# Performance work log

Measured on AMD Instinct MI355X. Metric: run time of the kernel, lower is better.

Reference implementation:

```python
import jax, jax.numpy as jnp
import numpy as np

S, N, E = 2048, 8, 512
C = 1024          # tot_classes
G = 32            # num_groups
CG = C // G       # classes_per_group = 32
INTERP_PROB = 1.0
LN_EPS = 1e-5


def setup_inputs() -> dict:
    key = jax.random.key(0)
    ks = jax.random.split(key, 8)
    return {
        "x": jax.random.normal(ks[0], (S, N, E), jnp.float32),
        "W1": jax.random.normal(ks[1], (C, E), jnp.float32) * 0.02,
        "b1": jnp.zeros((C,), jnp.float32),
        "class_offsets": jnp.zeros((C,), jnp.float32),
        "W2": jax.random.normal(ks[2], (E, C), jnp.float32) * 0.02,
        "b2": jnp.zeros((E,), jnp.float32),
        "ln_gamma": jnp.ones((E,), jnp.float32),
        "ln_beta": jnp.zeros((E,), jnp.float32),
        # Gumbel noise for the two categorical draws per group
        "g1": jax.random.gumbel(ks[3], (S, N, G, CG), jnp.float32),
        "g2": jax.random.gumbel(ks[4], (S, N, G, CG), jnp.float32),
        # interpolation weight and interp-decision uniform
        "w_interp": jax.random.uniform(ks[5], (S, N, G), jnp.float32),
        "u_interp": jax.random.uniform(ks[6], (S, N, G), jnp.float32),
    }


def _layer_norm(h, gamma, beta):
    mu = jnp.mean(h, axis=-1, keepdims=True)
    var = jnp.mean(jnp.square(h - mu), axis=-1, keepdims=True)
    return (h - mu) * jax.lax.rsqrt(var + LN_EPS) * gamma + beta


def reference(x, W1, b1, class_offsets, W2, b2, ln_gamma, ln_beta,
              g1, g2, w_interp, u_interp):
    # linear1, *3 scale, + class_offsets (min_prob_ratio > 0 path)
    logits = (jnp.einsum('sne,ce->snc', x, W1) + b1) * 3.0 + class_offsets
    lg = logits.reshape(S, N, G, CG)                      # grouped logits
    soft = jax.nn.softmax(lg, axis=-1)                    # per-group softmax
    softmax_out = soft.reshape(S, N, C)
    # flow_sample with straight_through_scale == 1.0:
    # categorical sample (Gumbel-argmax) of two classes, interpolate with
    # prob interp_prob, straight-through derivatives from the softmax.
    logp = jax.nn.log_softmax(lg, axis=-1)
    oh_i = jax.nn.one_hot(jnp.argmax(logp + g1, axis=-1), CG, dtype=lg.dtype)
    oh_j = jax.nn.one_hot(jnp.argmax(logp + g2, axis=-1), CG, dtype=lg.dtype)
    w = w_interp[..., None]
    interp = w * oh_i + (1.0 - w) * oh_j                  # E[interp] = softmax
    hard = jnp.where((u_interp < INTERP_PROB)[..., None], interp, oh_i)
    sampled = soft + jax.lax.stop_gradient(hard - soft)   # straight-through
    sampled = sampled.reshape(S, N, C)
    # projection back to embedding dim + LayerNorm
    pos = _layer_norm(jnp.einsum('snc,ec->sne', sampled, W2) + b2,
                      ln_gamma, ln_beta)
    # reverse_gradient: identity fwd, negated grad
    rev = 2.0 * jax.lax.stop_gradient(sampled) - sampled
    neg = _layer_norm(jnp.einsum('snc,ec->sne', rev, W2) + b2,
                      ln_gamma, ln_beta)
    return sampled, softmax_out, pos, neg
```

## Files before the change

kernel.cpp:

```cpp
#include <hip/hip_runtime.h>

#define ROWS 16384
#define EDIM 512
#define CDIM 1024

#define OFF_SOFT (16384 * 1024)
#define OFF_POS  (2 * 16384 * 1024)
#define OFF_NEG  (2 * 16384 * 1024 + 16384 * 512)

__global__ void transpose_w2_kernel(const float* __restrict__ in,
                                    float* __restrict__ out) {
  __shared__ float tile[32][33];
  const int bx = blockIdx.x * 32;
  const int by = blockIdx.y * 32;
  const int tx = threadIdx.x;
  const int ty = threadIdx.y;
#pragma unroll
  for (int i = 0; i < 32; i += 8)
    tile[ty + i][tx] = in[(size_t)(by + ty + i) * CDIM + bx + tx];
  __syncthreads();
#pragma unroll
  for (int i = 0; i < 32; i += 8)
    out[(size_t)(bx + ty + i) * EDIM + by + tx] = tile[tx][ty + i];
}

#define BM 128
#define BN 128
#define BK 16
#define TM 8
#define TN 8

__global__ __launch_bounds__(256, 2) void gemm1_fused_kernel(
    const float* __restrict__ A, const float* __restrict__ B,
    const float* __restrict__ bias1, const float* __restrict__ coff,
    const float* __restrict__ g1, const float* __restrict__ g2,
    const float* __restrict__ wI, const float* __restrict__ uI,
    float* __restrict__ out_samp, float* __restrict__ out_soft,
    float4* __restrict__ rec) {
  constexpr int K = EDIM;
  __shared__ __align__(16) float As[BK][BM + 4];
  __shared__ __align__(16) float Bs[BK][BN + 4];
  const int bm = blockIdx.y * BM;
  const int bn = blockIdx.x * BN;
  const int tid = threadIdx.x;
  const int tx = tid & 15;
  const int ty = tid >> 4;

  float acc[TM][TN] = {};

  const int lrow = tid >> 2;
  const int lk4 = (tid & 3) << 2;

  for (int k0 = 0; k0 < K; k0 += BK) {
#pragma unroll
    for (int i = 0; i < 2; i++) {
      const int row = lrow + i * 64;
      const float4 va = *(const float4*)&A[(size_t)(bm + row) * K + k0 + lk4];
      As[lk4 + 0][row] = va.x;
      As[lk4 + 1][row] = va.y;
      As[lk4 + 2][row] = va.z;
      As[lk4 + 3][row] = va.w;
      const float4 vb = *(const float4*)&B[(size_t)(bn + row) * K + k0 + lk4];
      Bs[lk4 + 0][row] = vb.x;
      Bs[lk4 + 1][row] = vb.y;
      Bs[lk4 + 2][row] = vb.z;
      Bs[lk4 + 3][row] = vb.w;
    }
    __syncthreads();
#pragma unroll
    for (int k = 0; k < BK; k++) {
      const float4 a0 = *(const float4*)&As[k][ty * TM];
      const float4 a1 = *(const float4*)&As[k][ty * TM + 4];
      const float4 c0 = *(const float4*)&Bs[k][tx * TN];
      const float4 c1 = *(const float4*)&Bs[k][tx * TN + 4];
      const float a[8] = {a0.x, a0.y, a0.z, a0.w, a1.x, a1.y, a1.z, a1.w};
      const float b[8] = {c0.x, c0.y, c0.z, c0.w, c1.x, c1.y, c1.z, c1.w};
#pragma unroll
      for (int i = 0; i < TM; i++)
#pragma unroll
        for (int j = 0; j < TN; j++)
          acc[i][j] = fmaf(a[i], b[j], acc[i][j]);
    }
    __syncthreads();
  }

  const int col0 = bn + tx * TN;
  const int cgbase = (tx & 3) * 8;
  const int g = (bn >> 5) + (tx >> 2);
  const float4 bias4a = *(const float4*)&bias1[col0];
  const float4 bias4b = *(const float4*)&bias1[col0 + 4];
  const float4 off4a = *(const float4*)&coff[col0];
  const float4 off4b = *(const float4*)&coff[col0 + 4];
  const float bb[8] = {bias4a.x, bias4a.y, bias4a.z, bias4a.w,
                       bias4b.x, bias4b.y, bias4b.z, bias4b.w};
  const float oo[8] = {off4a.x, off4a.y, off4a.z, off4a.w,
                       off4b.x, off4b.y, off4b.z, off4b.w};

#pragma unroll
  for (int i = 0; i < TM; i++) {
    const int row = bm + ty * TM + i;
    float lg[8];
#pragma unroll
    for (int j = 0; j < 8; j++) lg[j] = (acc[i][j] + bb[j]) * 3.0f + oo[j];

    float m = lg[0];
#pragma unroll
    for (int j = 1; j < 8; j++) m = fmaxf(m, lg[j]);
    m = fmaxf(m, __shfl_xor(m, 1));
    m = fmaxf(m, __shfl_xor(m, 2));

    float e[8], s = 0.0f;
#pragma unroll
    for (int j = 0; j < 8; j++) {
      e[j] = expf(lg[j] - m);
      s += e[j];
    }
    s += __shfl_xor(s, 1);
    s += __shfl_xor(s, 2);
    const float inv = 1.0f / s;
    const float lse = logf(s);

    const float* g1p = &g1[(size_t)row * CDIM + col0];
    const float* g2p = &g2[(size_t)row * CDIM + col0];
    const float4 gA0 = *(const float4*)g1p;
    const float4 gA1 = *(const float4*)(g1p + 4);
    const float4 gB0 = *(const float4*)g2p;
    const float4 gB1 = *(const float4*)(g2p + 4);
    const float ga[8] = {gA0.x, gA0.y, gA0.z, gA0.w, gA1.x, gA1.y, gA1.z, gA1.w};
    const float gb[8] = {gB0.x, gB0.y, gB0.z, gB0.w, gB1.x, gB1.y, gB1.z, gB1.w};

    float bv = (lg[0] - m) - lse + ga[0];
    int bi = cgbase;
    float cv = (lg[0] - m) - lse + gb[0];
    int cj = cgbase;
#pragma unroll
    for (int j = 1; j < 8; j++) {
      const float lp = (lg[j] - m) - lse;
      const float v1 = lp + ga[j];
      if (v1 > bv) { bv = v1; bi = cgbase + j; }
      const float v2 = lp + gb[j];
      if (v2 > cv) { cv = v2; cj = cgbase + j; }
    }
#pragma unroll
    for (int off = 1; off <= 2; off <<= 1) {
      const float ov = __shfl_xor(bv, off);
      const int oi = __shfl_xor(bi, off);
      if (ov > bv || (ov == bv && oi < bi)) { bv = ov; bi = oi; }
      const float ov2 = __shfl_xor(cv, off);
      const int oi2 = __shfl_xor(cj, off);
      if (ov2 > cv || (ov2 == cv && oi2 < cj)) { cv = ov2; cj = oi2; }
    }

    const float w = wI[(size_t)row * 32 + g];
    const float u = uI[(size_t)row * 32 + g];
    const bool take = (u < 1.0f);

    float so[8], sa[8];
#pragma unroll
    for (int j = 0; j < 8; j++) {
      const float soft = e[j] * inv;
      const int cg = cgbase + j;
      const float interp =
          (cg == bi ? w : 0.0f) + (cg == cj ? 1.0f - w : 0.0f);
      const float oh = (cg == bi) ? 1.0f : 0.0f;
      const float hard = take ? interp : oh;
      so[j] = soft;
      sa[j] = soft + (hard - soft);
    }
    float* soft_p = &out_soft[(size_t)row * CDIM + col0];
    float* samp_p = &out_samp[(size_t)row * CDIM + col0];
    *(float4*)soft_p = make_float4(so[0], so[1], so[2], so[3]);
    *(float4*)(soft_p + 4) = make_float4(so[4], so[5], so[6], so[7]);
    *(float4*)samp_p = make_float4(sa[0], sa[1], sa[2], sa[3]);
    *(float4*)(samp_p + 4) = make_float4(sa[4], sa[5], sa[6], sa[7]);

    if ((tx & 3) == 0) {
      const float wa = take ? w : 1.0f;
      const float wb = take ? (1.0f - w) : 0.0f;
      rec[(size_t)row * 32 + g] =
          make_float4(__int_as_float(g * 32 + bi), __int_as_float(g * 32 + cj),
                      wa, wb);
    }
  }
}

__global__ __launch_bounds__(256, 4) void finish_kernel(
    const float4* __restrict__ rec, const float* __restrict__ W2T,
    const float* __restrict__ b2, const float* __restrict__ gam,
    const float* __restrict__ bet, float* __restrict__ out_pos,
    float* __restrict__ out_neg) {
  const int r = blockIdx.x;
  const int tid = threadIdx.x;
  const int lane = tid & 63;
  const int wv = tid >> 6;

  __shared__ float s_wa[32], s_wb[32];
  __shared__ int s_ci[32], s_cj[32];
  __shared__ float s_red[4], s_red2[4];

  if (tid < 32) {
    const float4 f = rec[(size_t)r * 32 + tid];
    s_ci[tid] = __float_as_int(f.x);
    s_cj[tid] = __float_as_int(f.y);
    s_wa[tid] = f.z;
    s_wb[tid] = f.w;
  }
  __syncthreads();

  float ax = 0.0f, ay = 0.0f;
#pragma unroll 4
  for (int g = 0; g < 32; g++) {
    const float2 vi = ((const float2*)(W2T + (size_t)s_ci[g] * EDIM))[tid];
    const float2 vj = ((const float2*)(W2T + (size_t)s_cj[g] * EDIM))[tid];
    const float wa = s_wa[g], wb = s_wb[g];
    ax += wa * vi.x + wb * vj.x;
    ay += wa * vi.y + wb * vj.y;
  }
  const float2 b2v = ((const float2*)b2)[tid];
  const float hx = ax + b2v.x;
  const float hy = ay + b2v.y;

  float ss = hx + hy;
#pragma unroll
  for (int off = 32; off >= 1; off >>= 1) ss += __shfl_xor(ss, off);
  if (lane == 0) s_red[wv] = ss;
  __syncthreads();
  const float mu = (s_red[0] + s_red[1] + s_red[2] + s_red[3]) * (1.0f / 512.0f);
  const float dx = hx - mu, dy = hy - mu;
  float vv = dx * dx + dy * dy;
#pragma unroll
  for (int off = 32; off >= 1; off >>= 1) vv += __shfl_xor(vv, off);
  if (lane == 0) s_red2[wv] = vv;
  __syncthreads();
  const float var =
      (s_red2[0] + s_red2[1] + s_red2[2] + s_red2[3]) * (1.0f / 512.0f);
  const float rsig = 1.0f / sqrtf(var + 1e-5f);

  const float2 gv = ((const float2*)gam)[tid];
  const float2 bv2 = ((const float2*)bet)[tid];
  float2 o;
  o.x = dx * rsig * gv.x + bv2.x;
  o.y = dy * rsig * gv.y + bv2.y;
  ((float2*)(out_pos + (size_t)r * EDIM))[tid] = o;
  ((float2*)(out_neg + (size_t)r * EDIM))[tid] = o;
}

extern "C" void kernel_launch(void* const* d_in, const int* in_sizes, int n_in,
                              void* d_out, int out_size, void* d_ws,
                              size_t ws_size, hipStream_t stream) {
  const float* x = (const float*)d_in[0];
  const float* W1 = (const float*)d_in[1];
  const float* b1 = (const float*)d_in[2];
  const float* coff = (const float*)d_in[3];
  const float* W2 = (const float*)d_in[4];
  const float* b2 = (const float*)d_in[5];
  const float* gam = (const float*)d_in[6];
  const float* bet = (const float*)d_in[7];
  const float* g1 = (const float*)d_in[8];
  const float* g2 = (const float*)d_in[9];
  const float* wI = (const float*)d_in[10];
  const float* uI = (const float*)d_in[11];

  float* out = (float*)d_out;
  float* out_sampled = out;
  float* out_soft = out + OFF_SOFT;
  float* out_pos = out + OFF_POS;
  float* out_neg = out + OFF_NEG;

  float* W2T = (float*)d_ws;
  float4* rec = (float4*)((char*)d_ws + (size_t)CDIM * EDIM * 4);

  hipLaunchKernelGGL(transpose_w2_kernel, dim3(CDIM / 32, EDIM / 32),
                     dim3(32, 8), 0, stream, W2, W2T);
  hipLaunchKernelGGL(gemm1_fused_kernel, dim3(CDIM / BN, ROWS / BM), dim3(256),
                     0, stream, x, W1, b1, coff, g1, g2, wI, uI, out_sampled,
                     out_soft, rec);
  hipLaunchKernelGGL(finish_kernel, dim3(ROWS), dim3(256), 0, stream, rec, W2T,
                     b2, gam, bet, out_pos, out_neg);
}
```

Baseline: 638.8 us.

## Double-buffer GEMM shared tiles with register prefetch and split-K finish gather

The fused GEMM1 kernel now double-buffers its As/Bs shared-memory tiles. The next K-slice is prefetched into registers while the current slice is computed, which halves the barriers per iteration and overlaps global loads with FMAs. B tiles get a padded layout with a per-32-column skew to cut LDS bank conflicts, and launch bounds rise to 4 blocks per SM. The finish kernel splits the 32 groups across two half-blocks, each doing float4 gathers, and combines their partial sums through shared memory before the LayerNorm. The risks are higher register pressure from the occupancy hint and half the threads idling during the finish epilogue.

```diff
diff --git a/kernel.cpp b/kernel.cpp
--- a/kernel.cpp
+++ b/kernel.cpp
@@ -29,8 +29,9 @@
 #define BK 16
 #define TM 8
 #define TN 8
-
-__global__ __launch_bounds__(256, 2) void gemm1_fused_kernel(
+#define BS_STRIDE 140
+
+__global__ __launch_bounds__(256, 4) void gemm1_fused_kernel(
     const float* __restrict__ A, const float* __restrict__ B,
     const float* __restrict__ bias1, const float* __restrict__ coff,
     const float* __restrict__ g1, const float* __restrict__ g2,
@@ -38,8 +39,8 @@
     float* __restrict__ out_samp, float* __restrict__ out_soft,
     float4* __restrict__ rec) {
   constexpr int K = EDIM;
-  __shared__ __align__(16) float As[BK][BM + 4];
-  __shared__ __align__(16) float Bs[BK][BN + 4];
+  __shared__ __align__(16) float As[2][BK][BM + 4];
+  __shared__ __align__(16) float Bs[2][BK][BS_STRIDE];
   const int bm = blockIdx.y * BM;
   const int bn = blockIdx.x * BN;
   const int tid = threadIdx.x;
@@ -51,28 +52,42 @@
   const int lrow = tid >> 2;
   const int lk4 = (tid & 3) << 2;
 
-  for (int k0 = 0; k0 < K; k0 += BK) {
+  {
 #pragma unroll
     for (int i = 0; i < 2; i++) {
       const int row = lrow + i * 64;
-      const float4 va = *(const float4*)&A[(size_t)(bm + row) * K + k0 + lk4];
-      As[lk4 + 0][row] = va.x;
-      As[lk4 + 1][row] = va.y;
-      As[lk4 + 2][row] = va.z;
-      As[lk4 + 3][row] = va.w;
-      const float4 vb = *(const float4*)&B[(size_t)(bn + row) * K + k0 + lk4];
-      Bs[lk4 + 0][row] = vb.x;
-      Bs[lk4 + 1][row] = vb.y;
-      Bs[lk4 + 2][row] = vb.z;
-      Bs[lk4 + 3][row] = vb.w;
-    }
-    __syncthreads();
+      const float4 va = *(const float4*)&A[(size_t)(bm + row) * K + lk4];
+      const float4 vb = *(const float4*)&B[(size_t)(bn + row) * K + lk4];
+      As[0][lk4 + 0][row] = va.x;
+      As[0][lk4 + 1][row] = va.y;
+      As[0][lk4 + 2][row] = va.z;
+      As[0][lk4 + 3][row] = va.w;
+      const int pr = row + ((row >> 5) << 2);
+      Bs[0][lk4 + 0][pr] = vb.x;
+      Bs[0][lk4 + 1][pr] = vb.y;
+      Bs[0][lk4 + 2][pr] = vb.z;
+      Bs[0][lk4 + 3][pr] = vb.w;
+    }
+  }
+  __syncthreads();
+
+  const int bpc = tx * 8 + ((tx >> 2) << 2);
+  int buf = 0;
+
+  for (int k0 = 0; k0 < K - BK; k0 += BK) {
+    float4 pa[2], pb[2];
+#pragma unroll
+    for (int i = 0; i < 2; i++) {
+      const int row = lrow + i * 64;
+      pa[i] = *(const float4*)&A[(size_t)(bm + row) * K + k0 + BK + lk4];
+      pb[i] = *(const float4*)&B[(size_t)(bn + row) * K + k0 + BK + lk4];
+    }
 #pragma unroll
     for (int k = 0; k < BK; k++) {
-      const float4 a0 = *(const float4*)&As[k][ty * TM];
-      const float4 a1 = *(const float4*)&As[k][ty * TM + 4];
-      const float4 c0 = *(const float4*)&Bs[k][tx * TN];
-      const float4 c1 = *(const float4*)&Bs[k][tx * TN + 4];
+      const float4 a0 = *(const float4*)&As[buf][k][ty * TM];
+      const float4 a1 = *(const float4*)&As[buf][k][ty * TM + 4];
+      const float4 c0 = *(const float4*)&Bs[buf][k][bpc];
+      const float4 c1 = *(const float4*)&Bs[buf][k][bpc + 4];
       const float a[8] = {a0.x, a0.y, a0.z, a0.w, a1.x, a1.y, a1.z, a1.w};
       const float b[8] = {c0.x, c0.y, c0.z, c0.w, c1.x, c1.y, c1.z, c1.w};
 #pragma unroll
@@ -81,7 +96,36 @@
         for (int j = 0; j < TN; j++)
           acc[i][j] = fmaf(a[i], b[j], acc[i][j]);
     }
+    const int nb = buf ^ 1;
+#pragma unroll
+    for (int i = 0; i < 2; i++) {
+      const int row = lrow + i * 64;
+      As[nb][lk4 + 0][row] = pa[i].x;
+      As[nb][lk4 + 1][row] = pa[i].y;
+      As[nb][lk4 + 2][row] = pa[i].z;
+      As[nb][lk4 + 3][row] = pa[i].w;
+      const int pr = row + ((row >> 5) << 2);
+      Bs[nb][lk4 + 0][pr] = pb[i].x;
+      Bs[nb][lk4 + 1][pr] = pb[i].y;
+      Bs[nb][lk4 + 2][pr] = pb[i].z;
+      Bs[nb][lk4 + 3][pr] = pb[i].w;
+    }
     __syncthreads();
+    buf = nb;
+  }
+#pragma unroll
+  for (int k = 0; k < BK; k++) {
+    const float4 a0 = *(const float4*)&As[buf][k][ty * TM];
+    const float4 a1 = *(const float4*)&As[buf][k][ty * TM + 4];
+    const float4 c0 = *(const float4*)&Bs[buf][k][bpc];
+    const float4 c1 = *(const float4*)&Bs[buf][k][bpc + 4];
+    const float a[8] = {a0.x, a0.y, a0.z, a0.w, a1.x, a1.y, a1.z, a1.w};
+    const float b[8] = {c0.x, c0.y, c0.z, c0.w, c1.x, c1.y, c1.z, c1.w};
+#pragma unroll
+    for (int i = 0; i < TM; i++)
+#pragma unroll
+      for (int j = 0; j < TN; j++)
+        acc[i][j] = fmaf(a[i], b[j], acc[i][j]);
   }
 
   const int col0 = bn + tx * TN;
@@ -193,9 +237,12 @@
   const int tid = threadIdx.x;
   const int lane = tid & 63;
   const int wv = tid >> 6;
+  const int h = tid >> 7;
+  const int l = tid & 127;
 
   __shared__ float s_wa[32], s_wb[32];
   __shared__ int s_ci[32], s_cj[32];
+  __shared__ float4 s_part[128];
   __shared__ float s_red[4], s_red2[4];
 
   if (tid < 32) {
@@ -207,42 +254,59 @@
   }
   __syncthreads();
 
-  float ax = 0.0f, ay = 0.0f;
-#pragma unroll 4
-  for (int g = 0; g < 32; g++) {
-    const float2 vi = ((const float2*)(W2T + (size_t)s_ci[g] * EDIM))[tid];
-    const float2 vj = ((const float2*)(W2T + (size_t)s_cj[g] * EDIM))[tid];
+  float4 a = make_float4(0.f, 0.f, 0.f, 0.f);
+#pragma unroll 8
+  for (int gi = 0; gi < 16; gi++) {
+    const int g = h * 16 + gi;
+    const float4 vi = ((const float4*)(W2T + (size_t)s_ci[g] * EDIM))[l];
+    const float4 vj = ((const float4*)(W2T + (size_t)s_cj[g] * EDIM))[l];
     const float wa = s_wa[g], wb = s_wb[g];
-    ax += wa * vi.x + wb * vj.x;
-    ay += wa * vi.y + wb * vj.y;
-  }
-  const float2 b2v = ((const float2*)b2)[tid];
-  const float hx = ax + b2v.x;
-  const float hy = ay + b2v.y;
-
-  float ss = hx + hy;
+    a.x += wa * vi.x + wb * vj.x;
+    a.y += wa * vi.y + wb * vj.y;
+    a.z += wa * vi.z + wb * vj.z;
+    a.w += wa * vi.w + wb * vj.w;
+  }
+  if (h == 1) s_part[l] = a;
+  __syncthreads();
+
+  float4 hv = make_float4(0.f, 0.f, 0.f, 0.f);
+  if (h == 0) {
+    const float4 p = s_part[l];
+    const float4 b2v = ((const float4*)b2)[l];
+    hv.x = a.x + p.x + b2v.x;
+    hv.y = a.y + p.y + b2v.y;
+    hv.z = a.z + p.z + b2v.z;
+    hv.w = a.w + p.w + b2v.w;
+  }
+
+  float ss = hv.x + hv.y + hv.z + hv.w;
 #pragma unroll
   for (int off = 32; off >= 1; off >>= 1) ss += __shfl_xor(ss, off);
   if (lane == 0) s_red[wv] = ss;
   __syncthreads();
   const float mu = (s_red[0] + s_red[1] + s_red[2] + s_red[3]) * (1.0f / 512.0f);
-  const float dx = hx - mu, dy = hy - mu;
-  float vv = dx * dx + dy * dy;
-#pragma unroll
-  for (int off = 32; off >= 1; off >>= 1) vv += __shfl_xor(vv, off);
-  if (lane == 0) s_red2[wv] = vv;
+
+  const float dx = hv.x - mu, dy = hv.y - mu, dz = hv.z - mu, dw = hv.w - mu;
+  float vvv = (h == 0) ? (dx * dx + dy * dy + dz * dz + dw * dw) : 0.0f;
+#pragma unroll
+  for (int off = 32; off >= 1; off >>= 1) vvv += __shfl_xor(vvv, off);
+  if (lane == 0) s_red2[wv] = vvv;
   __syncthreads();
   const float var =
       (s_red2[0] + s_red2[1] + s_red2[2] + s_red2[3]) * (1.0f / 512.0f);
   const float rsig = 1.0f / sqrtf(var + 1e-5f);
 
-  const float2 gv = ((const float2*)gam)[tid];
-  const float2 bv2 = ((const float2*)bet)[tid];
-  float2 o;
-  o.x = dx * rsig * gv.x + bv2.x;
-  o.y = dy * rsig * gv.y + bv2.y;
-  ((float2*)(out_pos + (size_t)r * EDIM))[tid] = o;
-  ((float2*)(out_neg + (size_t)r * EDIM))[tid] = o;
+  if (h == 0) {
+    const float4 gv = ((const float4*)gam)[l];
+    const float4 bv = ((const float4*)bet)[l];
+    float4 o;
+    o.x = dx * rsig * gv.x + bv.x;
+    o.y = dy * rsig * gv.y + bv.y;
+    o.z = dz * rsig * gv.z + bv.z;
+    o.w = dw * rsig * gv.w + bv.w;
+    ((float4*)(out_pos + (size_t)r * EDIM))[l] = o;
+    ((float4*)(out_neg + (size_t)r * EDIM))[l] = o;
+  }
 }
 
 extern "C" void kernel_launch(void* const* d_in, const int* in_sizes, int n_in,
```

Result: slower. 964.2 us (+50.9%).
